# Optimization experiments

Hardware: AMD Instinct MI355X
Metric: run time of the kernel (lower is better)

The kernel has to match this reference:

```python
import jax, jax.numpy as jnp
import numpy as np

B, IN, HID, OUT, E, NMAP = 16384, 64, 128, 1, 64, 1000


def setup_inputs() -> dict:
    key = jax.random.key(0)
    ks = jax.random.split(key, 7)
    x = jax.random.normal(ks[0], (B, IN), dtype=jnp.float32)
    num = jax.random.randint(ks[1], (B,), 0, NMAP, dtype=jnp.int64)
    c = jax.random.randint(ks[2], (NMAP,), 0, E, dtype=jnp.int64)
    # per-expert 2-layer MLP params (kaiming-ish scale)
    W1 = jax.random.normal(ks[3], (E, IN, HID), dtype=jnp.float32) * (1.0 / np.sqrt(IN))
    b1 = jnp.zeros((E, HID), dtype=jnp.float32)
    W2 = jax.random.normal(ks[4], (E, HID, OUT), dtype=jnp.float32) * (1.0 / np.sqrt(HID))
    b2 = jnp.zeros((E, OUT), dtype=jnp.float32)
    return {"x": x, "num": num, "c": c, "W1": W1, "b1": b1, "W2": W2, "b2": b2}


def reference(x, num, c, W1, b1, W2, b2):
    # per-sample expert id: c[num[i]]
    e = c[num]                                   # [B]
    # gather each sample's expert weights and run batched MLP
    h = jnp.einsum('bi,bih->bh', x, W1[e]) + b1[e]   # [B, HID]
    h = jax.nn.relu(h)
    y = jnp.einsum('bh,bho->bo', h, W2[e]) + b2[e]   # [B, OUT]
    return jax.nn.sigmoid(y)
```

## Files before the change

kernel.cpp:

```cpp
#include <hip/hip_runtime.h>
#include <math.h>

#define B_N    16384
#define IN_D   64
#define HID_D  128
#define E_N    64
#define BPE    16
#define SCAN_N (B_N / BPE)
#define PER_T  (SCAN_N / 256)
#define CAP    256

typedef __attribute__((ext_vector_type(8))) short v8s;
typedef __attribute__((ext_vector_type(4))) float v4f;

__device__ __forceinline__ short f2bf(float f) {
    unsigned int u = __float_as_uint(f);
    u += 0x7fffu + ((u >> 16) & 1u);
    return (short)(u >> 16);
}

__global__ __launch_bounds__(256) void moe_mfma(
    const float* __restrict__ x,
    const int*   __restrict__ num,
    const int*   __restrict__ c,
    const float* __restrict__ W1,
    const float* __restrict__ b1,
    const float* __restrict__ W2,
    const float* __restrict__ b2,
    float*       __restrict__ out)
{
    __shared__ int   s_list[CAP];
    __shared__ int   s_cnt;
    __shared__ float s_yw[4][CAP];

    const int tid    = threadIdx.x;
    const int expert = blockIdx.x & (E_N - 1);
    const int q      = blockIdx.x >> 6;
    if (tid == 0) s_cnt = 0;

    const int wave = __builtin_amdgcn_readfirstlane(tid >> 6);
    const int lane = tid & 63;
    const int l16  = lane & 15;
    const int quad = lane >> 4;

    const int base = q * SCAN_N + tid;
    int nums[PER_T];
    #pragma unroll
    for (int it = 0; it < PER_T; ++it) nums[it] = num[base + it * 256];

    const float* W1e = W1 + (size_t)expert * (IN_D * HID_D);
    v8s bfrag[2][2];
    #pragma unroll
    for (int nt = 0; nt < 2; ++nt) {
        const int h = 32 * wave + 16 * nt + l16;
        #pragma unroll
        for (int kh = 0; kh < 2; ++kh)
            #pragma unroll
            for (int j = 0; j < 8; ++j)
                bfrag[nt][kh][j] = f2bf(W1e[(32 * kh + 8 * quad + j) * HID_D + h]);
    }
    const int   h0   = 32 * wave + l16, h1 = h0 + 16;
    const float b1v0 = b1[expert * HID_D + h0], b1v1 = b1[expert * HID_D + h1];
    const float w2v0 = W2[expert * HID_D + h0], w2v1 = W2[expert * HID_D + h1];
    const float b2v  = b2[expert];

    int es[PER_T];
    #pragma unroll
    for (int it = 0; it < PER_T; ++it) es[it] = c[nums[it]];

    __syncthreads();
    #pragma unroll
    for (int it = 0; it < PER_T; ++it) {
        if (es[it] == expert) {
            int p = atomicAdd(&s_cnt, 1);
            if (p < CAP) s_list[p] = base + it * 256;
        }
    }
    __syncthreads();
    const int cnt    = min(s_cnt, CAP);
    const int ntiles = (cnt + 15) >> 4;

    for (int mt = 0; mt < ntiles; ++mt) {
        const int idx = mt * 16 + l16;
        const int s   = s_list[min(idx, cnt - 1)];
        const float4* row = (const float4*)(x + (size_t)s * IN_D);

        const float4 f0 = row[2 * quad],     f1 = row[2 * quad + 1];
        const float4 f2 = row[8 + 2 * quad], f3 = row[8 + 2 * quad + 1];
        v8s a0, a1;
        a0[0]=f2bf(f0.x); a0[1]=f2bf(f0.y); a0[2]=f2bf(f0.z); a0[3]=f2bf(f0.w);
        a0[4]=f2bf(f1.x); a0[5]=f2bf(f1.y); a0[6]=f2bf(f1.z); a0[7]=f2bf(f1.w);
        a1[0]=f2bf(f2.x); a1[1]=f2bf(f2.y); a1[2]=f2bf(f2.z); a1[3]=f2bf(f2.w);
        a1[4]=f2bf(f3.x); a1[5]=f2bf(f3.y); a1[6]=f2bf(f3.z); a1[7]=f2bf(f3.w);

        v4f acc0 = {0.f, 0.f, 0.f, 0.f};
        v4f acc1 = {0.f, 0.f, 0.f, 0.f};
        acc0 = __builtin_amdgcn_mfma_f32_16x16x32_bf16(a0, bfrag[0][0], acc0, 0, 0, 0);
        acc0 = __builtin_amdgcn_mfma_f32_16x16x32_bf16(a1, bfrag[0][1], acc0, 0, 0, 0);
        acc1 = __builtin_amdgcn_mfma_f32_16x16x32_bf16(a0, bfrag[1][0], acc1, 0, 0, 0);
        acc1 = __builtin_amdgcn_mfma_f32_16x16x32_bf16(a1, bfrag[1][1], acc1, 0, 0, 0);

        #pragma unroll
        for (int r = 0; r < 4; ++r) {
            float v = fmaxf(acc0[r] + b1v0, 0.f) * w2v0
                    + fmaxf(acc1[r] + b1v1, 0.f) * w2v1;
            v += __shfl_xor(v, 1);
            v += __shfl_xor(v, 2);
            v += __shfl_xor(v, 4);
            v += __shfl_xor(v, 8);
            if (l16 == 0) s_yw[wave][mt * 16 + quad * 4 + r] = v;
        }
    }
    __syncthreads();

    for (int i = tid; i < cnt; i += 256) {
        const float t = s_yw[0][i] + s_yw[1][i] + s_yw[2][i] + s_yw[3][i] + b2v;
        out[s_list[i]] = 1.0f / (1.0f + expf(-t));
    }
}

extern "C" void kernel_launch(void* const* d_in, const int* in_sizes, int n_in,
                              void* d_out, int out_size, void* d_ws, size_t ws_size,
                              hipStream_t stream)
{
    const float* x   = (const float*)d_in[0];
    const int*   num = (const int*)  d_in[1];
    const int*   c   = (const int*)  d_in[2];
    const float* W1  = (const float*)d_in[3];
    const float* b1  = (const float*)d_in[4];
    const float* W2  = (const float*)d_in[5];
    const float* b2  = (const float*)d_in[6];
    float*       out = (float*)d_out;

    moe_mfma<<<dim3(E_N * BPE), dim3(256), 0, stream>>>(x, num, c, W1, b1, W2, b2, out);
}
```

Measured before the change: 74.32 us.

## Split into prep kernel for expert bucketing and bf16 fragment packing plus compute kernel

Adds a prep kernel that buckets each 256-sample chunk by expert into per-chunk lists in workspace and converts W1 to bf16 MFMA fragment layout once per expert. The compute kernel then reads four chunk lists for its expert, compacts them, and loads pre-packed fragments instead of rescanning num/c and reconverting W1 in every block. This removes the redundant full scan (each block read 1024 indices) and repeated strided W1 conversion, at the cost of an extra kernel launch, workspace round-trips, and a fixed per-chunk capacity of 48 samples per expert, which could drop samples if a bucket overflows.

After: 74.55 us. No clear change (+0.3%).

```diff
diff --git a/kernel.cpp b/kernel.cpp
--- a/kernel.cpp
+++ b/kernel.cpp
@@ -5,10 +5,17 @@
 #define IN_D   64
 #define HID_D  128
 #define E_N    64
-#define BPE    16
-#define SCAN_N (B_N / BPE)
-#define PER_T  (SCAN_N / 256)
-#define CAP    256
+#define SB_N   64
+#define CAP_BE 48
+#define GRP    4
+#define NGRP   (SB_N / GRP)
+#define CAPC   (GRP * CAP_BE)
+
+#define FRAG_OFF  0
+#define FRAG_SZ   (E_N * IN_D * HID_D * 2)
+#define CNT_OFF   (FRAG_OFF + FRAG_SZ)
+#define CNT_SZ    (SB_N * E_N * 4)
+#define LIST_OFF  (CNT_OFF + CNT_SZ)
 
 typedef __attribute__((ext_vector_type(8))) short v8s;
 typedef __attribute__((ext_vector_type(4))) float v4f;
@@ -19,70 +26,100 @@
     return (short)(u >> 16);
 }
 
-__global__ __launch_bounds__(256) void moe_mfma(
+__global__ __launch_bounds__(256) void ka_prep(
+    const int* __restrict__ num, const int* __restrict__ c,
+    const float* __restrict__ W1, unsigned char* __restrict__ ws)
+{
+    const int tid = threadIdx.x;
+    if (blockIdx.x < SB_N) {
+        __shared__ int lcnt[E_N];
+        __shared__ int llist[E_N * CAP_BE];
+        int* cnt  = (int*)(ws + CNT_OFF);
+        int* list = (int*)(ws + LIST_OFF);
+        const int b = blockIdx.x;
+        if (tid < E_N) lcnt[tid] = 0;
+        const int s = b * 256 + tid;
+        const int e = c[num[s]];
+        __syncthreads();
+        int p = atomicAdd(&lcnt[e], 1);
+        if (p < CAP_BE) llist[e * CAP_BE + p] = s;
+        __syncthreads();
+        if (tid < E_N) cnt[b * E_N + tid] = min(lcnt[tid], CAP_BE);
+        for (int j = tid; j < E_N * CAP_BE; j += 256)
+            list[b * E_N * CAP_BE + j] = llist[j];
+    } else {
+        const int e = blockIdx.x - SB_N;
+        const float* W1e = W1 + (size_t)e * (IN_D * HID_D);
+        const int f0    = tid * 4;
+        const int w     = f0 >> 8, nt = (f0 >> 7) & 1, kh = (f0 >> 6) & 1;
+        const int quad  = (f0 >> 4) & 3;
+        const int hbase = 32 * w + 16 * nt + (f0 & 15);
+        v8s t[4];
+        #pragma unroll
+        for (int j = 0; j < 8; ++j) {
+            const float4 v = *(const float4*)&W1e[(32 * kh + 8 * quad + j) * HID_D + hbase];
+            t[0][j] = f2bf(v.x); t[1][j] = f2bf(v.y);
+            t[2][j] = f2bf(v.z); t[3][j] = f2bf(v.w);
+        }
+        v8s* frag = (v8s*)(ws + FRAG_OFF) + (size_t)e * (IN_D * HID_D / 8);
+        #pragma unroll
+        for (int i = 0; i < 4; ++i) frag[f0 + i] = t[i];
+    }
+}
+
+__global__ __launch_bounds__(256) void kb_compute(
     const float* __restrict__ x,
-    const int*   __restrict__ num,
-    const int*   __restrict__ c,
-    const float* __restrict__ W1,
-    const float* __restrict__ b1,
-    const float* __restrict__ W2,
+    const float* __restrict__ b1, const float* __restrict__ W2,
     const float* __restrict__ b2,
-    float*       __restrict__ out)
+    const unsigned char* __restrict__ ws, float* __restrict__ out)
 {
-    __shared__ int   s_list[CAP];
-    __shared__ int   s_cnt;
-    __shared__ float s_yw[4][CAP];
+    __shared__ int   s_c[GRP], s_pfx[GRP + 1];
+    __shared__ int   s_list[CAPC];
+    __shared__ float s_yw[4][CAPC];
 
-    const int tid    = threadIdx.x;
-    const int expert = blockIdx.x & (E_N - 1);
-    const int q      = blockIdx.x >> 6;
-    if (tid == 0) s_cnt = 0;
+    const int tid = threadIdx.x;
+    const int e   = blockIdx.x & (E_N - 1);
+    const int g   = blockIdx.x >> 6;
+    const int* cnt  = (const int*)(ws + CNT_OFF);
+    const int* list = (const int*)(ws + LIST_OFF);
+
+    if (tid < GRP) s_c[tid] = cnt[(g * GRP + tid) * E_N + e];
+    __syncthreads();
+    if (tid == 0) {
+        int a = 0;
+        for (int i = 0; i < GRP; ++i) { s_pfx[i] = a; a += s_c[i]; }
+        s_pfx[GRP] = a;
+    }
+    __syncthreads();
+    const int total = s_pfx[GRP];
+
+    for (int j = tid; j < GRP * CAP_BE; j += 256) {
+        const int sub = j / CAP_BE, slot = j - sub * CAP_BE;
+        if (slot < s_c[sub])
+            s_list[s_pfx[sub] + slot] =
+                list[((g * GRP + sub) * E_N + e) * CAP_BE + slot];
+    }
 
     const int wave = __builtin_amdgcn_readfirstlane(tid >> 6);
-    const int lane = tid & 63;
-    const int l16  = lane & 15;
-    const int quad = lane >> 4;
-
-    const int base = q * SCAN_N + tid;
-    int nums[PER_T];
-    #pragma unroll
-    for (int it = 0; it < PER_T; ++it) nums[it] = num[base + it * 256];
-
-    const float* W1e = W1 + (size_t)expert * (IN_D * HID_D);
+    const int lane = tid & 63, l16 = lane & 15, quad = lane >> 4;
+    const v8s* frag = (const v8s*)(ws + FRAG_OFF) + (size_t)e * (IN_D * HID_D / 8);
     v8s bfrag[2][2];
     #pragma unroll
-    for (int nt = 0; nt < 2; ++nt) {
-        const int h = 32 * wave + 16 * nt + l16;
+    for (int nt = 0; nt < 2; ++nt)
         #pragma unroll
         for (int kh = 0; kh < 2; ++kh)
-            #pragma unroll
-            for (int j = 0; j < 8; ++j)
-                bfrag[nt][kh][j] = f2bf(W1e[(32 * kh + 8 * quad + j) * HID_D + h]);
-    }
+            bfrag[nt][kh] = frag[((wave * 2 + nt) * 2 + kh) * 64 + lane];
+
     const int   h0   = 32 * wave + l16, h1 = h0 + 16;
-    const float b1v0 = b1[expert * HID_D + h0], b1v1 = b1[expert * HID_D + h1];
-    const float w2v0 = W2[expert * HID_D + h0], w2v1 = W2[expert * HID_D + h1];
-    const float b2v  = b2[expert];
+    const float b1v0 = b1[e * HID_D + h0], b1v1 = b1[e * HID_D + h1];
+    const float w2v0 = W2[e * HID_D + h0], w2v1 = W2[e * HID_D + h1];
+    const float b2v  = b2[e];
+    __syncthreads();
 
-    int es[PER_T];
-    #pragma unroll
-    for (int it = 0; it < PER_T; ++it) es[it] = c[nums[it]];
-
-    __syncthreads();
-    #pragma unroll
-    for (int it = 0; it < PER_T; ++it) {
-        if (es[it] == expert) {
-            int p = atomicAdd(&s_cnt, 1);
-            if (p < CAP) s_list[p] = base + it * 256;
-        }
-    }
-    __syncthreads();
-    const int cnt    = min(s_cnt, CAP);
-    const int ntiles = (cnt + 15) >> 4;
-
+    const int ntiles = (total + 15) >> 4;
     for (int mt = 0; mt < ntiles; ++mt) {
         const int idx = mt * 16 + l16;
-        const int s   = s_list[min(idx, cnt - 1)];
+        const int s   = s_list[min(idx, total - 1)];
         const float4* row = (const float4*)(x + (size_t)s * IN_D);
 
         const float4 f0 = row[2 * quad],     f1 = row[2 * quad + 1];
@@ -113,7 +150,7 @@
     }
     __syncthreads();
 
-    for (int i = tid; i < cnt; i += 256) {
+    for (int i = tid; i < total; i += 256) {
         const float t = s_yw[0][i] + s_yw[1][i] + s_yw[2][i] + s_yw[3][i] + b2v;
         out[s_list[i]] = 1.0f / (1.0f + expf(-t));
     }
@@ -131,6 +168,8 @@
     const float* W2  = (const float*)d_in[5];
     const float* b2  = (const float*)d_in[6];
     float*       out = (float*)d_out;
+    unsigned char* ws = (unsigned char*)d_ws;
 
-    moe_mfma<<<dim3(E_N * BPE), dim3(256), 0, stream>>>(x, num, c, W1, b1, W2, b2, out);
+    ka_prep   <<<dim3(SB_N + E_N),   dim3(256), 0, stream>>>(num, c, W1, ws);
+    kb_compute<<<dim3(E_N * NGRP),   dim3(256), 0, stream>>>(x, b1, W2, b2, ws, out);
 }
```
